# Optimization experiments

Hardware: AMD Instinct MI355X
Metric: run time of the kernel (lower is better)

Reference implementation:

```python
import jax, jax.numpy as jnp
import numpy as np

D = 256      # layer_size
BLOCK = 4096 # block_size


def setup_inputs() -> dict:
    key = jax.random.key(0)
    ks = jax.random.split(key, 7)
    B, T = 4, BLOCK
    x = jax.random.normal(ks[0], (B, T, D), dtype=jnp.float32)
    s = 1.0 / np.sqrt(D)
    Wq = jax.random.uniform(ks[1], (D, D), jnp.float32, -s, s)
    bq = jax.random.uniform(ks[2], (D,), jnp.float32, -s, s)
    Wk = jax.random.uniform(ks[3], (D, D), jnp.float32, -s, s)
    bk = jax.random.uniform(ks[4], (D,), jnp.float32, -s, s)
    Wv = jax.random.uniform(ks[5], (D, D), jnp.float32, -s, s)
    bv = jax.random.uniform(ks[6], (D,), jnp.float32, -s, s)
    return {"x": x, "Wq": Wq, "bq": bq, "Wk": Wk, "bk": bk, "Wv": Wv, "bv": bv}


def reference(x, Wq, bq, Wk, bk, Wv, bv):
    # x: [B, T, D]; Linear uses x @ W.T + b (torch convention)
    B, T, _ = x.shape
    Q = x @ Wq.T + bq
    K = x @ Wk.T + bk
    V = x @ Wv.T + bv
    scores = jnp.einsum('btd,bsd->bts', Q, K) / jnp.sqrt(jnp.float32(D))  # [B,T,T]
    # causal mask buffer is [1,1,T,T]; torch masked_fill broadcasts it against
    # [B,T,T] scores, yielding [1,B,T,T] — reproduce that shape faithfully.
    causal = jnp.tril(jnp.ones((T, T), dtype=bool))[None, None]  # [1,1,T,T]
    scores = jnp.where(causal, scores, -jnp.inf)                 # [1,B,T,T]
    attn = jax.nn.softmax(scores, axis=-1)                       # [1,B,T,T]
    out = jnp.einsum('abts,bsd->abtd', attn, V)                  # [1,B,T,D]
    return out
```

## Files before the change

### kernel.cpp

```cpp
#include <hip/hip_runtime.h>
#include <hip/hip_bf16.h>

typedef __attribute__((ext_vector_type(8))) short short8;
typedef __attribute__((ext_vector_type(4))) short short4v;
typedef __attribute__((ext_vector_type(4))) float f32x4;

#define MFMA16(a, b, c) __builtin_amdgcn_mfma_f32_16x16x32_bf16(a, b, c, 0, 0, 0)

__device__ __forceinline__ short f2bf(float f) {
    union { float f; unsigned u; } v; v.f = f;
    unsigned r = v.u + 0x7fffu + ((v.u >> 16) & 1u);
    return (short)(r >> 16);
}
__device__ __forceinline__ unsigned pack2(float lo, float hi) {
    return ((unsigned)(unsigned short)f2bf(hi) << 16) |
           (unsigned)(unsigned short)f2bf(lo);
}
__device__ __forceinline__ void gload16(const void* g, void* lds) {
    __builtin_amdgcn_global_load_lds(
        (const __attribute__((address_space(1))) unsigned int*)g,
        (__attribute__((address_space(3))) unsigned int*)lds, 16, 0, 0);
}

__global__ __launch_bounds__(256) void wconv(
    const float* __restrict__ Wq, const float* __restrict__ Wk,
    const float* __restrict__ Wv, short* __restrict__ Wb)
{
    int e = (blockIdx.x * 256 + threadIdx.x) * 8;
    const float* p = (e < 65536) ? (Wq + e)
                   : (e < 131072) ? (Wk + (e - 65536))
                                  : (Wv + (e - 131072));
    float4 a = *(const float4*)p;
    float4 b = *(const float4*)(p + 4);
    short8 h = { f2bf(a.x), f2bf(a.y), f2bf(a.z), f2bf(a.w),
                 f2bf(b.x), f2bf(b.y), f2bf(b.z), f2bf(b.w) };
    *(short8*)(Wb + e) = h;
}

__global__ __launch_bounds__(256) void qkv_proj(
    const float* __restrict__ x, const short* __restrict__ Wb,
    const float* __restrict__ bq, const float* __restrict__ bk,
    const float* __restrict__ bv,
    short* __restrict__ Qb, short* __restrict__ Kb, short* __restrict__ VTg)
{
    __shared__ short xs[64 * 264];
    __shared__ short wsS[64 * 264];

    const int tid = threadIdx.x;
    const int wid = tid >> 6;
    const int l   = tid & 63;
    const int l15 = l & 15, lg = l >> 4;
    const int r0  = blockIdx.x * 64;
    const int cg  = blockIdx.y;

    {
        const float4* src = (const float4*)(x + (size_t)r0 * 256);
        #pragma unroll
        for (int p = 0; p < 16; ++p) {
            float4 v = src[p * 256 + tid];
            int idx = (p * 256 + tid) * 4;
            int row = idx >> 8, col = idx & 255;
            short4v h = { f2bf(v.x), f2bf(v.y), f2bf(v.z), f2bf(v.w) };
            *(short4v*)&xs[row * 264 + col] = h;
        }
    }

    short8 wreg[8];
    {
        const short8* wsrc = (const short8*)(Wb + (size_t)(cg * 3) * 64 * 256);
        #pragma unroll
        for (int p = 0; p < 8; ++p) wreg[p] = wsrc[p * 256 + tid];
    }
    __syncthreads();

    short8 afr[8];
    {
        const int arow = wid * 16 + l15;
        #pragma unroll
        for (int ks = 0; ks < 8; ++ks)
            afr[ks] = *(const short8*)&xs[arow * 264 + ks * 32 + lg * 8];
    }

    const float* bm[3] = { bq, bk, bv };

    for (int c = 0; c < 3; ++c) {
        const int gc  = cg * 3 + c;
        const int m   = gc >> 2;
        const int wr0 = (gc & 3) * 64;

        #pragma unroll
        for (int p = 0; p < 8; ++p) {
            int idx8 = p * 256 + tid;
            int row = idx8 >> 5, col = (idx8 & 31) * 8;
            *(short8*)&wsS[row * 264 + col] = wreg[p];
        }
        __syncthreads();

        if (c < 2) {
            const short8* wsrc =
                (const short8*)(Wb + (size_t)(gc + 1) * 64 * 256);
            #pragma unroll
            for (int p = 0; p < 8; ++p) wreg[p] = wsrc[p * 256 + tid];
        }

        f32x4 acc[4] = {};
        #pragma unroll
        for (int n = 0; n < 4; ++n) {
            const short* kr = &wsS[(n * 16 + l15) * 264 + lg * 8];
            #pragma unroll
            for (int ks = 0; ks < 8; ++ks) {
                short8 bfr = *(const short8*)(kr + ks * 32);
                acc[n] = MFMA16(afr[ks], bfr, acc[n]);
            }
        }

        const int rowbase = r0 + wid * 16 + (lg << 2);
        #pragma unroll
        for (int n = 0; n < 4; ++n) {
            const int col   = wr0 + n * 16 + l15;
            const float bias = bm[m][col];
            #pragma unroll
            for (int j = 0; j < 4; ++j) {
                const int grow = rowbase + j;
                short hv = f2bf(acc[n][j] + bias);
                if (m == 0)      Qb[(size_t)grow * 256 + col] = hv;
                else if (m == 1) Kb[(size_t)grow * 256 + col] = hv;
                else {
                    int bb = grow >> 12, tt = grow & 4095;
                    VTg[(size_t)bb * (256 * 4096) + (size_t)col * 4096 + tt] = hv;
                }
            }
        }
        __syncthreads();
    }
}

__global__ __launch_bounds__(512, 1) void attn_fwd(
    const short* __restrict__ Qb, const short* __restrict__ Kb,
    const short* __restrict__ VTg, float* __restrict__ out)
{
    __shared__ __attribute__((aligned(16))) char SMEM[143360];
    short* Ps = (short*)(SMEM + 131072);

    const int tid = threadIdx.x;
    const int wid = tid >> 6;
    const int l   = tid & 63;
    const int l15 = l & 15, lg = l >> 4;
    const int rg  = wid >> 2;
    const int par = wid & 3;

    const int bid    = blockIdx.x;
    const int rowblk = 127 - (bid >> 2);
    const int b      = bid & 3;
    const int nkt    = rowblk + 1;
    const int nsi    = (nkt + 3) >> 2;

    const short* KbB = Kb  + (size_t)b * 4096 * 256;
    const short* VTB = VTg + (size_t)b * (256 * 4096);

    const int qrow_loc = rg * 16 + l15;
    const int qrow     = rowblk * 32 + qrow_loc;

    short8 qf[8];
    {
        const short* qr = Qb + ((size_t)(b * 4096 + qrow)) * 256 + lg * 8;
        #pragma unroll
        for (int ks = 0; ks < 8; ++ks)
            qf[ks] = *(const short8*)(qr + ks * 32);
    }

    auto stage = [&](int si) {
        const int ktt = si * 4 + (wid & 3);
        if (ktt >= nkt) return;
        if (wid < 4) {
            char* lb = SMEM + (wid & 3) * 16384;
            const short* gK = KbB + (size_t)ktt * 32 * 256;
            #pragma unroll
            for (int inst = 0; inst < 16; ++inst) {
                int off  = inst * 1024 + l * 16;
                int key  = off >> 9;
                int slot = ((off >> 4) & 31) ^ (key & 15);
                gload16(gK + key * 256 + slot * 8, lb + inst * 1024);
            }
        } else {
            char* lb = SMEM + 65536 + (wid & 3) * 16384;
            const short* gV = VTB + ktt * 32;
            #pragma unroll
            for (int inst = 0; inst < 16; ++inst) {
                int off = inst * 1024 + l * 16;
                int d   = off >> 6;
                int s   = ((off >> 4) & 3) ^ ((d >> 1) & 3);
                gload16(gV + (size_t)d * 4096 + s * 8, lb + inst * 1024);
            }
        }
    };
    stage(0);

    f32x4 o[16] = {};
    float mrow = -INFINITY, srow = 0.f;

    for (int si = 0; si < nsi; ++si) {
        asm volatile("s_waitcnt vmcnt(0)" ::: "memory");
        __syncthreads();

        const int kt  = si * 4 + par;
        const bool act = (kt < nkt);
        short8 vf2[4], pb;
        float  f;

        if (act) {
            const short* Kt = (const short*)(SMEM + par * 16384);
            f32x4 sA[2] = {};
            #pragma unroll
            for (int tk = 0; tk < 2; ++tk) {
                const int key = tk * 16 + l15;
                #pragma unroll
                for (int ks = 0; ks < 8; ++ks) {
                    const int slot = (ks * 4 + lg) ^ l15;
                    short8 kf = *(const short8*)(Kt + key * 256 + slot * 8);
                    sA[tk] = MFMA16(kf, qf[ks], sA[tk]);
                }
            }

            float pmax = -INFINITY;
            #pragma unroll
            for (int tk = 0; tk < 2; ++tk)
                #pragma unroll
                for (int j4 = 0; j4 < 4; ++j4) {
                    const int key = kt * 32 + tk * 16 + lg * 4 + j4;
                    float v = sA[tk][j4] * 0.0625f;
                    v = (key > qrow) ? -INFINITY : v;
                    sA[tk][j4] = v;
                    pmax = fmaxf(pmax, v);
                }
            pmax = fmaxf(pmax, __shfl_xor(pmax, 16, 64));
            pmax = fmaxf(pmax, __shfl_xor(pmax, 32, 64));

            const float mn  = fmaxf(mrow, pmax);
            const float mne = (mn == -INFINITY) ? 0.f : mn;
            f = __expf(mrow - mne);
            mrow = mn;

            short* Pw = Ps + wid * 768;
            float ps = 0.f;
            #pragma unroll
            for (int tk = 0; tk < 2; ++tk) {
                float p0 = __expf(sA[tk][0] - mne);
                float p1 = __expf(sA[tk][1] - mne);
                float p2 = __expf(sA[tk][2] - mne);
                float p3 = __expf(sA[tk][3] - mne);
                ps += (p0 + p1) + (p2 + p3);
                unsigned* pw = (unsigned*)(Pw + l15 * 48 + tk * 16 + lg * 4);
                pw[0] = pack2(p0, p1);
                pw[1] = pack2(p2, p3);
            }
            srow = srow * f + ps;

            asm volatile("s_waitcnt lgkmcnt(0)" ::: "memory");
            __builtin_amdgcn_sched_barrier(0);

            pb = *(const short8*)(Pw + l15 * 48 + lg * 8);

            const short* Vt = (const short*)(SMEM + 65536 + par * 16384);
            #pragma unroll
            for (int dt = 0; dt < 12; ++dt) {
                #pragma unroll
                for (int j4 = 0; j4 < 4; ++j4) o[dt][j4] *= f;
                const int d  = dt * 16 + l15;
                const int sx = lg ^ ((d >> 1) & 3);
                short8 va = *(const short8*)(Vt + d * 32 + sx * 8);
                o[dt] = MFMA16(va, pb, o[dt]);
            }
            #pragma unroll
            for (int dt = 12; dt < 16; ++dt) {
                const int d  = dt * 16 + l15;
                const int sx = lg ^ ((d >> 1) & 3);
                vf2[dt - 12] = *(const short8*)(Vt + d * 32 + sx * 8);
            }
        }

        __syncthreads();
        if (si + 1 < nsi) stage(si + 1);
        __builtin_amdgcn_sched_barrier(0);

        if (act) {
            #pragma unroll
            for (int dt = 12; dt < 16; ++dt) {
                #pragma unroll
                for (int j4 = 0; j4 < 4; ++j4) o[dt][j4] *= f;
                o[dt] = MFMA16(vf2[dt - 12], pb, o[dt]);
            }
        }
    }

    srow += __shfl_xor(srow, 16, 64);
    srow += __shfl_xor(srow, 32, 64);

    __syncthreads();
    float* scr = (float*)SMEM;
    float* ms  = (float*)(SMEM + 66560);

    const int rl = rg * 16 + l15;

    if (par >= 2) {
        const int p = par - 2;
        #pragma unroll
        for (int dt = 0; dt < 16; ++dt)
            *(f32x4*)&scr[p * 8320 + rl * 260 + dt * 16 + lg * 4] = o[dt];
        if (lg == 0) {
            ms[p * 64 + rl * 2 + 0] = mrow;
            ms[p * 64 + rl * 2 + 1] = srow;
        }
    }
    __syncthreads();
    if (par < 2) {
        const float m1 = ms[par * 64 + rl * 2 + 0];
        const float s1 = ms[par * 64 + rl * 2 + 1];
        const float M  = fmaxf(mrow, m1);
        const float Me = (M == -INFINITY) ? 0.f : M;
        const float w0 = __expf(mrow - Me);
        const float w1 = __expf(m1 - Me);
        srow = srow * w0 + s1 * w1;
        mrow = M;
        #pragma unroll
        for (int dt = 0; dt < 16; ++dt) {
            f32x4 o1 = *(f32x4*)&scr[par * 8320 + rl * 260 + dt * 16 + lg * 4];
            #pragma unroll
            for (int j4 = 0; j4 < 4; ++j4)
                o[dt][j4] = o[dt][j4] * w0 + o1[j4] * w1;
        }
    }
    __syncthreads();
    if (par == 1) {
        #pragma unroll
        for (int dt = 0; dt < 16; ++dt)
            *(f32x4*)&scr[rl * 260 + dt * 16 + lg * 4] = o[dt];
        if (lg == 0) {
            ms[rl * 2 + 0] = mrow;
            ms[rl * 2 + 1] = srow;
        }
    }
    __syncthreads();
    if (par == 0) {
        const float m1 = ms[rl * 2 + 0];
        const float s1 = ms[rl * 2 + 1];
        const float M  = fmaxf(mrow, m1);
        const float Me = (M == -INFINITY) ? 0.f : M;
        const float w0 = __expf(mrow - Me);
        const float w1 = __expf(m1 - Me);
        const float rs = 1.f / (srow * w0 + s1 * w1);
        float* og = out + ((size_t)(b * 4096 + rowblk * 32 + rl)) * 256;
        #pragma unroll
        for (int dt = 0; dt < 16; ++dt) {
            f32x4 o1 = *(f32x4*)&scr[rl * 260 + dt * 16 + lg * 4];
            f32x4 r;
            #pragma unroll
            for (int j4 = 0; j4 < 4; ++j4)
                r[j4] = (o[dt][j4] * w0 + o1[j4] * w1) * rs;
            *(f32x4*)&og[dt * 16 + lg * 4] = r;
        }
    }
}

extern "C" void kernel_launch(void* const* d_in, const int* in_sizes, int n_in,
                              void* d_out, int out_size, void* d_ws, size_t ws_size,
                              hipStream_t stream) {
    const float* x  = (const float*)d_in[0];
    const float* Wq = (const float*)d_in[1];
    const float* bq = (const float*)d_in[2];
    const float* Wk = (const float*)d_in[3];
    const float* bk = (const float*)d_in[4];
    const float* Wv = (const float*)d_in[5];
    const float* bv = (const float*)d_in[6];

    short* Qb  = (short*)d_ws;
    short* Kb  = Qb + (size_t)16384 * 256;
    short* VTg = Kb + (size_t)16384 * 256;
    short* Wb  = VTg + (size_t)4 * 256 * 4096;
    float* out = (float*)d_out;

    wconv<<<dim3(96), dim3(256), 0, stream>>>(Wq, Wk, Wv, Wb);
    qkv_proj<<<dim3(256, 4), dim3(256), 0, stream>>>(x, Wb, bq, bk, bv,
                                                     Qb, Kb, VTg);
    attn_fwd<<<dim3(512), dim3(512), 0, stream>>>(Qb, Kb, VTg, out);
}
```

Measured before the change: 144.6 us.

## Split attention into 16-row blocks with per-wave K staging and direct V loads

Attention work moves from 32-row blocks of 8 waves to 16-row blocks of 4 waves (1024 blocks, 2 per CU). Each wave now streams its own K tiles into a private LDS buffer without block-wide barriers in the main loop. V fragments are read straight from global memory instead of being staged through LDS. The aim is to remove __syncthreads stalls, raise occupancy and balance work better across CUs. The trade-off is that the 16 uncoalesced V loads per tile may raise global memory latency and traffic, and K tiles are no longer shared across two row groups.

```diff
diff --git a/kernel.cpp b/kernel.cpp
--- a/kernel.cpp
+++ b/kernel.cpp
@@ -135,31 +135,29 @@
     }
 }
 
-__global__ __launch_bounds__(512, 1) void attn_fwd(
+__global__ __launch_bounds__(256, 2) void attn_fwd(
     const short* __restrict__ Qb, const short* __restrict__ Kb,
     const short* __restrict__ VTg, float* __restrict__ out)
 {
-    __shared__ __attribute__((aligned(16))) char SMEM[143360];
-    short* Ps = (short*)(SMEM + 131072);
+    __shared__ __attribute__((aligned(16))) char SMEM[71680];
+    short* Ps = (short*)(SMEM + 65536);
 
     const int tid = threadIdx.x;
     const int wid = tid >> 6;
     const int l   = tid & 63;
     const int l15 = l & 15, lg = l >> 4;
-    const int rg  = wid >> 2;
-    const int par = wid & 3;
+    const int par = wid;
 
     const int bid    = blockIdx.x;
-    const int rowblk = 127 - (bid >> 2);
+    const int rowblk = 255 - (bid >> 2);
     const int b      = bid & 3;
-    const int nkt    = rowblk + 1;
-    const int nsi    = (nkt + 3) >> 2;
+    const int nkt    = (rowblk >> 1) + 1;
+    const int nsiw   = (nkt > par) ? ((nkt - par + 3) >> 2) : 0;
 
     const short* KbB = Kb  + (size_t)b * 4096 * 256;
     const short* VTB = VTg + (size_t)b * (256 * 4096);
 
-    const int qrow_loc = rg * 16 + l15;
-    const int qrow     = rowblk * 32 + qrow_loc;
+    const int qrow = rowblk * 16 + l15;
 
     short8 qf[8];
     {
@@ -169,29 +167,17 @@
             qf[ks] = *(const short8*)(qr + ks * 32);
     }
 
+    char* Kbuf = SMEM + wid * 16384;
     auto stage = [&](int si) {
-        const int ktt = si * 4 + (wid & 3);
+        const int ktt = 4 * si + par;
         if (ktt >= nkt) return;
-        if (wid < 4) {
-            char* lb = SMEM + (wid & 3) * 16384;
-            const short* gK = KbB + (size_t)ktt * 32 * 256;
-            #pragma unroll
-            for (int inst = 0; inst < 16; ++inst) {
-                int off  = inst * 1024 + l * 16;
-                int key  = off >> 9;
-                int slot = ((off >> 4) & 31) ^ (key & 15);
-                gload16(gK + key * 256 + slot * 8, lb + inst * 1024);
-            }
-        } else {
-            char* lb = SMEM + 65536 + (wid & 3) * 16384;
-            const short* gV = VTB + ktt * 32;
-            #pragma unroll
-            for (int inst = 0; inst < 16; ++inst) {
-                int off = inst * 1024 + l * 16;
-                int d   = off >> 6;
-                int s   = ((off >> 4) & 3) ^ ((d >> 1) & 3);
-                gload16(gV + (size_t)d * 4096 + s * 8, lb + inst * 1024);
-            }
+        const short* gK = KbB + (size_t)ktt * 32 * 256;
+        #pragma unroll
+        for (int inst = 0; inst < 16; ++inst) {
+            int off  = inst * 1024 + l * 16;
+            int key  = off >> 9;
+            int slot = ((off >> 4) & 31) ^ (key & 15);
+            gload16(gK + key * 256 + slot * 8, Kbuf + inst * 1024);
         }
     };
     stage(0);
@@ -199,97 +185,75 @@
     f32x4 o[16] = {};
     float mrow = -INFINITY, srow = 0.f;
 
-    for (int si = 0; si < nsi; ++si) {
+    for (int si = 0; si < nsiw; ++si) {
+        const int kt = 4 * si + par;
+
         asm volatile("s_waitcnt vmcnt(0)" ::: "memory");
-        __syncthreads();
-
-        const int kt  = si * 4 + par;
-        const bool act = (kt < nkt);
-        short8 vf2[4], pb;
-        float  f;
-
-        if (act) {
-            const short* Kt = (const short*)(SMEM + par * 16384);
-            f32x4 sA[2] = {};
-            #pragma unroll
-            for (int tk = 0; tk < 2; ++tk) {
-                const int key = tk * 16 + l15;
-                #pragma unroll
-                for (int ks = 0; ks < 8; ++ks) {
-                    const int slot = (ks * 4 + lg) ^ l15;
-                    short8 kf = *(const short8*)(Kt + key * 256 + slot * 8);
-                    sA[tk] = MFMA16(kf, qf[ks], sA[tk]);
-                }
+        __builtin_amdgcn_sched_barrier(0);
+
+        const short* Kt = (const short*)Kbuf;
+        f32x4 sA[2] = {};
+        #pragma unroll
+        for (int tk = 0; tk < 2; ++tk) {
+            const int key = tk * 16 + l15;
+            #pragma unroll
+            for (int ks = 0; ks < 8; ++ks) {
+                const int slot = (ks * 4 + lg) ^ l15;
+                short8 kf = *(const short8*)(Kt + key * 256 + slot * 8);
+                sA[tk] = MFMA16(kf, qf[ks], sA[tk]);
             }
-
-            float pmax = -INFINITY;
-            #pragma unroll
-            for (int tk = 0; tk < 2; ++tk)
-                #pragma unroll
-                for (int j4 = 0; j4 < 4; ++j4) {
-                    const int key = kt * 32 + tk * 16 + lg * 4 + j4;
-                    float v = sA[tk][j4] * 0.0625f;
-                    v = (key > qrow) ? -INFINITY : v;
-                    sA[tk][j4] = v;
-                    pmax = fmaxf(pmax, v);
-                }
-            pmax = fmaxf(pmax, __shfl_xor(pmax, 16, 64));
-            pmax = fmaxf(pmax, __shfl_xor(pmax, 32, 64));
-
-            const float mn  = fmaxf(mrow, pmax);
-            const float mne = (mn == -INFINITY) ? 0.f : mn;
-            f = __expf(mrow - mne);
-            mrow = mn;
-
-            short* Pw = Ps + wid * 768;
-            float ps = 0.f;
-            #pragma unroll
-            for (int tk = 0; tk < 2; ++tk) {
-                float p0 = __expf(sA[tk][0] - mne);
-                float p1 = __expf(sA[tk][1] - mne);
-                float p2 = __expf(sA[tk][2] - mne);
-                float p3 = __expf(sA[tk][3] - mne);
-                ps += (p0 + p1) + (p2 + p3);
-                unsigned* pw = (unsigned*)(Pw + l15 * 48 + tk * 16 + lg * 4);
-                pw[0] = pack2(p0, p1);
-                pw[1] = pack2(p2, p3);
+        }
+
+        asm volatile("s_waitcnt lgkmcnt(0)" ::: "memory");
+        __builtin_amdgcn_sched_barrier(0);
+        stage(si + 1);
+
+        float pmax = -INFINITY;
+        #pragma unroll
+        for (int tk = 0; tk < 2; ++tk)
+            #pragma unroll
+            for (int j4 = 0; j4 < 4; ++j4) {
+                const int key = kt * 32 + tk * 16 + lg * 4 + j4;
+                float v = sA[tk][j4] * 0.0625f;
+                v = (key > qrow) ? -INFINITY : v;
+                sA[tk][j4] = v;
+                pmax = fmaxf(pmax, v);
             }
-            srow = srow * f + ps;
-
-            asm volatile("s_waitcnt lgkmcnt(0)" ::: "memory");
-            __builtin_amdgcn_sched_barrier(0);
-
-            pb = *(const short8*)(Pw + l15 * 48 + lg * 8);
-
-            const short* Vt = (const short*)(SMEM + 65536 + par * 16384);
-            #pragma unroll
-            for (int dt = 0; dt < 12; ++dt) {
-                #pragma unroll
-                for (int j4 = 0; j4 < 4; ++j4) o[dt][j4] *= f;
-                const int d  = dt * 16 + l15;
-                const int sx = lg ^ ((d >> 1) & 3);
-                short8 va = *(const short8*)(Vt + d * 32 + sx * 8);
-                o[dt] = MFMA16(va, pb, o[dt]);
-            }
-            #pragma unroll
-            for (int dt = 12; dt < 16; ++dt) {
-                const int d  = dt * 16 + l15;
-                const int sx = lg ^ ((d >> 1) & 3);
-                vf2[dt - 12] = *(const short8*)(Vt + d * 32 + sx * 8);
-            }
-        }
-
-        __syncthreads();
-        if (si + 1 < nsi) stage(si + 1);
+        pmax = fmaxf(pmax, __shfl_xor(pmax, 16, 64));
+        pmax = fmaxf(pmax, __shfl_xor(pmax, 32, 64));
+
+        const float mn  = fmaxf(mrow, pmax);
+        const float mne = (mn == -INFINITY) ? 0.f : mn;
+        const float f   = __expf(mrow - mne);
+        mrow = mn;
+
+        short* Pw = Ps + wid * 768;
+        float ps = 0.f;
+        #pragma unroll
+        for (int tk = 0; tk < 2; ++tk) {
+            float p0 = __expf(sA[tk][0] - mne);
+            float p1 = __expf(sA[tk][1] - mne);
+            float p2 = __expf(sA[tk][2] - mne);
+            float p3 = __expf(sA[tk][3] - mne);
+            ps += (p0 + p1) + (p2 + p3);
+            unsigned* pw = (unsigned*)(Pw + l15 * 48 + tk * 16 + lg * 4);
+            pw[0] = pack2(p0, p1);
+            pw[1] = pack2(p2, p3);
+        }
+        srow = srow * f + ps;
+
+        asm volatile("s_waitcnt lgkmcnt(0)" ::: "memory");
         __builtin_amdgcn_sched_barrier(0);
 
-        if (act) {
-            #pragma unroll
-            for (int dt = 12; dt < 16; ++dt) {
-                #pragma unroll
-                for (int j4 = 0; j4 < 4; ++j4) o[dt][j4] *= f;
-                o[dt] = MFMA16(vf2[dt - 12], pb, o[dt]);
-            }
+        const short8 pb = *(const short8*)(Pw + l15 * 48 + lg * 8);
+
+        const short* Vg = VTB + (size_t)kt * 32 + lg * 8;
+        #pragma unroll
+        for (int dt = 0; dt < 16; ++dt) {
+            #pragma unroll
+            for (int j4 = 0; j4 < 4; ++j4) o[dt][j4] *= f;
+            short8 va = *(const short8*)(Vg + (size_t)(dt * 16 + l15) * 4096);
+            o[dt] = MFMA16(va, pb, o[dt]);
         }
     }
 
@@ -298,24 +262,24 @@
 
     __syncthreads();
     float* scr = (float*)SMEM;
-    float* ms  = (float*)(SMEM + 66560);
-
-    const int rl = rg * 16 + l15;
+    float* ms  = (float*)(SMEM + 33280);
+
+    const int rl = l15;
 
     if (par >= 2) {
         const int p = par - 2;
         #pragma unroll
         for (int dt = 0; dt < 16; ++dt)
-            *(f32x4*)&scr[p * 8320 + rl * 260 + dt * 16 + lg * 4] = o[dt];
+            *(f32x4*)&scr[p * 4160 + rl * 260 + dt * 16 + lg * 4] = o[dt];
         if (lg == 0) {
-            ms[p * 64 + rl * 2 + 0] = mrow;
-            ms[p * 64 + rl * 2 + 1] = srow;
+            ms[p * 32 + rl * 2 + 0] = mrow;
+            ms[p * 32 + rl * 2 + 1] = srow;
         }
     }
     __syncthreads();
     if (par < 2) {
-        const float m1 = ms[par * 64 + rl * 2 + 0];
-        const float s1 = ms[par * 64 + rl * 2 + 1];
+        const float m1 = ms[par * 32 + rl * 2 + 0];
+        const float s1 = ms[par * 32 + rl * 2 + 1];
         const float M  = fmaxf(mrow, m1);
         const float Me = (M == -INFINITY) ? 0.f : M;
         const float w0 = __expf(mrow - Me);
@@ -324,7 +288,7 @@
         mrow = M;
         #pragma unroll
         for (int dt = 0; dt < 16; ++dt) {
-            f32x4 o1 = *(f32x4*)&scr[par * 8320 + rl * 260 + dt * 16 + lg * 4];
+            f32x4 o1 = *(f32x4*)&scr[par * 4160 + rl * 260 + dt * 16 + lg * 4];
             #pragma unroll
             for (int j4 = 0; j4 < 4; ++j4)
                 o[dt][j4] = o[dt][j4] * w0 + o1[j4] * w1;
@@ -349,7 +313,7 @@
         const float w0 = __expf(mrow - Me);
         const float w1 = __expf(m1 - Me);
         const float rs = 1.f / (srow * w0 + s1 * w1);
-        float* og = out + ((size_t)(b * 4096 + rowblk * 32 + rl)) * 256;
+        float* og = out + ((size_t)(b * 4096 + rowblk * 16 + rl)) * 256;
         #pragma unroll
         for (int dt = 0; dt < 16; ++dt) {
             f32x4 o1 = *(f32x4*)&scr[rl * 260 + dt * 16 + lg * 4];
@@ -382,5 +346,5 @@
     wconv<<<dim3(96), dim3(256), 0, stream>>>(Wq, Wk, Wv, Wb);
     qkv_proj<<<dim3(256, 4), dim3(256), 0, stream>>>(x, Wb, bq, bk, bv,
                                                      Qb, Kb, VTg);
-    attn_fwd<<<dim3(512), dim3(512), 0, stream>>>(Qb, Kb, VTg, out);
-}
+    attn_fwd<<<dim3(1024), dim3(256), 0, stream>>>(Qb, Kb, VTg, out);
+}
```

Result: slower. 200.2 us (+38.4%).

## Read V fragments directly from global memory and shrink LDS to only K tiles

Applied to the files above, without the earlier changes.

Stops staging V^T tiles in LDS. Each wave now loads its V fragments straight from global/L2 memory inside the PV loop, and all eight waves share the work of staging the K tiles. The shared-memory footprint drops from about 140KB to about 76KB, and launch bounds now ask for a higher occupancy hint. The stage call moves to right after the QK MFMAs. The intent is to free LDS, overlap the next K prefetch with softmax and PV, and remove the split PV loop. The cost is global-latency loads in the inner MFMA loop with no prefetch.

```diff
diff --git a/kernel.cpp b/kernel.cpp
--- a/kernel.cpp
+++ b/kernel.cpp
@@ -135,12 +135,12 @@
     }
 }
 
-__global__ __launch_bounds__(512, 1) void attn_fwd(
+__global__ __launch_bounds__(512, 4) void attn_fwd(
     const short* __restrict__ Qb, const short* __restrict__ Kb,
     const short* __restrict__ VTg, float* __restrict__ out)
 {
-    __shared__ __attribute__((aligned(16))) char SMEM[143360];
-    short* Ps = (short*)(SMEM + 131072);
+    __shared__ __attribute__((aligned(16))) char SMEM[77824];
+    short* Ps = (short*)(SMEM + 65536);
 
     const int tid = threadIdx.x;
     const int wid = tid >> 6;
@@ -172,26 +172,15 @@
     auto stage = [&](int si) {
         const int ktt = si * 4 + (wid & 3);
         if (ktt >= nkt) return;
-        if (wid < 4) {
-            char* lb = SMEM + (wid & 3) * 16384;
-            const short* gK = KbB + (size_t)ktt * 32 * 256;
-            #pragma unroll
-            for (int inst = 0; inst < 16; ++inst) {
-                int off  = inst * 1024 + l * 16;
-                int key  = off >> 9;
-                int slot = ((off >> 4) & 31) ^ (key & 15);
-                gload16(gK + key * 256 + slot * 8, lb + inst * 1024);
-            }
-        } else {
-            char* lb = SMEM + 65536 + (wid & 3) * 16384;
-            const short* gV = VTB + ktt * 32;
-            #pragma unroll
-            for (int inst = 0; inst < 16; ++inst) {
-                int off = inst * 1024 + l * 16;
-                int d   = off >> 6;
-                int s   = ((off >> 4) & 3) ^ ((d >> 1) & 3);
-                gload16(gV + (size_t)d * 4096 + s * 8, lb + inst * 1024);
-            }
+        char* lb = SMEM + (wid & 3) * 16384 + (wid >> 2) * 8192;
+        const short* gK = KbB + (size_t)ktt * 32 * 256;
+        const int base = (wid >> 2) * 8192;
+        #pragma unroll
+        for (int inst = 0; inst < 8; ++inst) {
+            int off  = base + inst * 1024 + l * 16;
+            int key  = off >> 9;
+            int slot = ((off >> 4) & 31) ^ (key & 15);
+            gload16(gK + key * 256 + slot * 8, lb + inst * 1024);
         }
     };
     stage(0);
@@ -205,12 +194,10 @@
 
         const int kt  = si * 4 + par;
         const bool act = (kt < nkt);
-        short8 vf2[4], pb;
-        float  f;
+        f32x4 sA[2] = {};
 
         if (act) {
             const short* Kt = (const short*)(SMEM + par * 16384);
-            f32x4 sA[2] = {};
             #pragma unroll
             for (int tk = 0; tk < 2; ++tk) {
                 const int key = tk * 16 + l15;
@@ -221,7 +208,12 @@
                     sA[tk] = MFMA16(kf, qf[ks], sA[tk]);
                 }
             }
-
+        }
+
+        __syncthreads();
+        if (si + 1 < nsi) stage(si + 1);
+
+        if (act) {
             float pmax = -INFINITY;
             #pragma unroll
             for (int tk = 0; tk < 2; ++tk)
@@ -238,7 +230,7 @@
 
             const float mn  = fmaxf(mrow, pmax);
             const float mne = (mn == -INFINITY) ? 0.f : mn;
-            f = __expf(mrow - mne);
+            const float f   = __expf(mrow - mne);
             mrow = mn;
 
             short* Pw = Ps + wid * 768;
@@ -259,36 +251,15 @@
             asm volatile("s_waitcnt lgkmcnt(0)" ::: "memory");
             __builtin_amdgcn_sched_barrier(0);
 
-            pb = *(const short8*)(Pw + l15 * 48 + lg * 8);
-
-            const short* Vt = (const short*)(SMEM + 65536 + par * 16384);
-            #pragma unroll
-            for (int dt = 0; dt < 12; ++dt) {
+            const short8 pb = *(const short8*)(Pw + l15 * 48 + lg * 8);
+
+            const short* Vg = VTB + (size_t)kt * 32 + lg * 8;
+            #pragma unroll
+            for (int dt = 0; dt < 16; ++dt) {
                 #pragma unroll
                 for (int j4 = 0; j4 < 4; ++j4) o[dt][j4] *= f;
-                const int d  = dt * 16 + l15;
-                const int sx = lg ^ ((d >> 1) & 3);
-                short8 va = *(const short8*)(Vt + d * 32 + sx * 8);
+                short8 va = *(const short8*)(Vg + (size_t)(dt * 16 + l15) * 4096);
                 o[dt] = MFMA16(va, pb, o[dt]);
-            }
-            #pragma unroll
-            for (int dt = 12; dt < 16; ++dt) {
-                const int d  = dt * 16 + l15;
-                const int sx = lg ^ ((d >> 1) & 3);
-                vf2[dt - 12] = *(const short8*)(Vt + d * 32 + sx * 8);
-            }
-        }
-
-        __syncthreads();
-        if (si + 1 < nsi) stage(si + 1);
-        __builtin_amdgcn_sched_barrier(0);
-
-        if (act) {
-            #pragma unroll
-            for (int dt = 12; dt < 16; ++dt) {
-                #pragma unroll
-                for (int j4 = 0; j4 < 4; ++j4) o[dt][j4] *= f;
-                o[dt] = MFMA16(vf2[dt - 12], pb, o[dt]);
             }
         }
     }
```

Measured after the change: 412.4 us. +185.2%, slower.

## Pre-convert x to bf16 and stage QKV projection tiles via async LDS loads

Applied to the files above, without the earlier changes.

Extends the weight conversion kernel so it also converts x to bf16 into workspace. A new projection kernel loads the bf16 x and weight tiles straight into swizzled LDS with global_load_lds, holds the A fragments in registers, and prefetches the next weight chunk while the current results are written out. It also raises occupancy to two blocks per CU. The aim is to cut the cost of converting fp32 x in the projection kernel and to hide load latency, at the cost of an extra full pass over x and a dependence on workspace size, with the old path kept as a fallback.

```diff
diff --git a/kernel.cpp b/kernel.cpp
--- a/kernel.cpp
+++ b/kernel.cpp
@@ -37,6 +37,32 @@
     *(short8*)(Wb + e) = h;
 }
 
+__global__ __launch_bounds__(256) void conv2(
+    const float* __restrict__ Wq, const float* __restrict__ Wk,
+    const float* __restrict__ Wv, const float* __restrict__ x,
+    short* __restrict__ Wb, short* __restrict__ xb)
+{
+    const int bid = blockIdx.x;
+    if (bid < 96) {
+        int e = (bid * 256 + threadIdx.x) * 8;
+        const float* p = (e < 65536) ? (Wq + e)
+                       : (e < 131072) ? (Wk + (e - 65536))
+                                      : (Wv + (e - 131072));
+        float4 a = *(const float4*)p;
+        float4 b = *(const float4*)(p + 4);
+        short8 h = { f2bf(a.x), f2bf(a.y), f2bf(a.z), f2bf(a.w),
+                     f2bf(b.x), f2bf(b.y), f2bf(b.z), f2bf(b.w) };
+        *(short8*)(Wb + e) = h;
+    } else {
+        int e = ((bid - 96) * 256 + threadIdx.x) * 8;
+        float4 a = *(const float4*)(x + e);
+        float4 b = *(const float4*)(x + e + 4);
+        short8 h = { f2bf(a.x), f2bf(a.y), f2bf(a.z), f2bf(a.w),
+                     f2bf(b.x), f2bf(b.y), f2bf(b.z), f2bf(b.w) };
+        *(short8*)(xb + e) = h;
+    }
+}
+
 __global__ __launch_bounds__(256) void qkv_proj(
     const float* __restrict__ x, const short* __restrict__ Wb,
     const float* __restrict__ bq, const float* __restrict__ bk,
@@ -131,6 +157,103 @@
                 }
             }
         }
+        __syncthreads();
+    }
+}
+
+__global__ __launch_bounds__(256, 2) void qkv_proj2(
+    const short* __restrict__ xb, const short* __restrict__ Wb,
+    const float* __restrict__ bq, const float* __restrict__ bk,
+    const float* __restrict__ bv,
+    short* __restrict__ Qb, short* __restrict__ Kb, short* __restrict__ VTg)
+{
+    __shared__ __attribute__((aligned(16))) char SM[65536];
+
+    const int tid = threadIdx.x;
+    const int wid = tid >> 6;
+    const int l   = tid & 63;
+    const int l15 = l & 15, lg = l >> 4;
+    const int r0  = blockIdx.x * 64;
+    const int cg  = blockIdx.y;
+
+    {
+        const short* gx = xb + (size_t)r0 * 256;
+        #pragma unroll
+        for (int inst = 0; inst < 8; ++inst) {
+            int off  = inst * 4096 + wid * 1024 + l * 16;
+            int row  = off >> 9;
+            int slot = ((off >> 4) & 31) ^ (row & 15);
+            gload16(gx + row * 256 + slot * 8, SM + inst * 4096 + wid * 1024);
+        }
+    }
+    auto stageW = [&](int c) {
+        if (c >= 3) return;
+        const short* gW = Wb + (size_t)(cg * 3 + c) * 64 * 256;
+        #pragma unroll
+        for (int inst = 0; inst < 8; ++inst) {
+            int off  = inst * 4096 + wid * 1024 + l * 16;
+            int row  = off >> 9;
+            int slot = ((off >> 4) & 31) ^ (row & 15);
+            gload16(gW + row * 256 + slot * 8,
+                    SM + 32768 + inst * 4096 + wid * 1024);
+        }
+    };
+    stageW(0);
+
+    asm volatile("s_waitcnt vmcnt(0)" ::: "memory");
+    __syncthreads();
+
+    short8 afr[8];
+    {
+        const int arow = wid * 16 + l15;
+        #pragma unroll
+        for (int ks = 0; ks < 8; ++ks) {
+            const int slot = (ks * 4 + lg) ^ l15;
+            afr[ks] = *(const short8*)(SM + arow * 512 + slot * 16);
+        }
+    }
+
+    const float* bm[3] = { bq, bk, bv };
+
+    for (int c = 0; c < 3; ++c) {
+        const int gc  = cg * 3 + c;
+        const int m   = gc >> 2;
+        const int wr0 = (gc & 3) * 64;
+
+        f32x4 acc[4] = {};
+        #pragma unroll
+        for (int n = 0; n < 4; ++n) {
+            const int brow = n * 16 + l15;
+            #pragma unroll
+            for (int ks = 0; ks < 8; ++ks) {
+                const int slot = (ks * 4 + lg) ^ l15;
+                short8 bfr = *(const short8*)(SM + 32768 + brow * 512 + slot * 16);
+                acc[n] = MFMA16(afr[ks], bfr, acc[n]);
+            }
+        }
+
+        __syncthreads();
+        stageW(c + 1);
+
+        const int rowbase = r0 + wid * 16 + (lg << 2);
+        #pragma unroll
+        for (int n = 0; n < 4; ++n) {
+            const int col   = wr0 + n * 16 + l15;
+            const float bias = bm[m][col];
+            #pragma unroll
+            for (int j = 0; j < 4; ++j) {
+                const int grow = rowbase + j;
+                short hv = f2bf(acc[n][j] + bias);
+                if (m == 0)      Qb[(size_t)grow * 256 + col] = hv;
+                else if (m == 1) Kb[(size_t)grow * 256 + col] = hv;
+                else {
+                    int bb = grow >> 12, tt = grow & 4095;
+                    VTg[(size_t)bb * (256 * 4096) + (size_t)col * 4096 + tt] = hv;
+                }
+            }
+        }
+
+        asm volatile("s_waitcnt vmcnt(0)" ::: "memory");
         __syncthreads();
     }
 }
@@ -377,10 +500,19 @@
     short* Kb  = Qb + (size_t)16384 * 256;
     short* VTg = Kb + (size_t)16384 * 256;
     short* Wb  = VTg + (size_t)4 * 256 * 4096;
+    short* xbb = Wb + (size_t)768 * 256;
     float* out = (float*)d_out;
 
-    wconv<<<dim3(96), dim3(256), 0, stream>>>(Wq, Wk, Wv, Wb);
-    qkv_proj<<<dim3(256, 4), dim3(256), 0, stream>>>(x, Wb, bq, bk, bv,
-                                                     Qb, Kb, VTg);
+    const bool fast = ws_size >= (size_t)33947648;
+
+    if (fast) {
+        conv2<<<dim3(2144), dim3(256), 0, stream>>>(Wq, Wk, Wv, x, Wb, xbb);
+        qkv_proj2<<<dim3(256, 4), dim3(256), 0, stream>>>(xbb, Wb, bq, bk, bv,
+                                                          Qb, Kb, VTg);
+    } else {
+        wconv<<<dim3(96), dim3(256), 0, stream>>>(Wq, Wk, Wv, Wb);
+        qkv_proj<<<dim3(256, 4), dim3(256), 0, stream>>>(x, Wb, bq, bk, bv,
+                                                         Qb, Kb, VTg);
+    }
     attn_fwd<<<dim3(512), dim3(512), 0, stream>>>(Qb, Kb, VTg, out);
 }
```

Result: faster. 138.0 us, median of 2 (-4.5%).
